# Performance work log

Measured on AMD Instinct MI355X. Metric: run time of the kernel, lower is better.

The kernel has to match this reference:

```python
import jax, jax.numpy as jnp
import numpy as np

B, NQ, NK, C = 8, 1024, 1024, 1024
H, DK, DV = 16, 64, 64


def setup_inputs() -> dict:
    key = jax.random.key(0)
    ks = jax.random.split(key, 10)
    queries = jax.random.normal(ks[0], (B, NQ, C), dtype=jnp.float32)
    keys_ = jax.random.normal(ks[1], (B, NK, C), dtype=jnp.float32)
    values = jax.random.normal(ks[2], (B, NK, C), dtype=jnp.float32)
    attention_mask = jax.random.randint(ks[3], (B, H, NQ, NK), 0, 2).astype(jnp.bool_)
    attention_weights = jax.random.uniform(ks[4], (B, H, NQ, NK), dtype=jnp.float32)
    std = 0.001  # init.normal_(m.weight, std=0.001), bias=0
    Wq = jax.random.normal(ks[5], (C, H * DK), dtype=jnp.float32) * std
    Wk = jax.random.normal(ks[6], (C, H * DK), dtype=jnp.float32) * std
    Wv = jax.random.normal(ks[7], (C, H * DV), dtype=jnp.float32) * std
    Wo = jax.random.normal(ks[8], (H * DV, C), dtype=jnp.float32) * std
    bq = jnp.zeros((H * DK,), jnp.float32)
    bk = jnp.zeros((H * DK,), jnp.float32)
    bv = jnp.zeros((H * DV,), jnp.float32)
    bo = jnp.zeros((C,), jnp.float32)
    return {"queries": queries, "keys": keys_, "values": values,
            "attention_mask": attention_mask, "attention_weights": attention_weights,
            "Wq": Wq, "bq": bq, "Wk": Wk, "bk": bk, "Wv": Wv, "bv": bv,
            "Wo": Wo, "bo": bo}


def reference(queries, keys, values, attention_mask, attention_weights,
              Wq, bq, Wk, bk, Wv, bv, Wo, bo):
    bs, nq, _ = queries.shape
    nk = keys.shape[1]
    # projections -> (b, h, n, d)
    q = (queries @ Wq + bq).reshape(bs, nq, H, DK).transpose(0, 2, 1, 3)
    k = (keys @ Wk + bk).reshape(bs, nk, H, DK).transpose(0, 2, 1, 3)
    v = (values @ Wv + bv).reshape(bs, nk, H, DV).transpose(0, 2, 1, 3)
    att = jnp.einsum('bhqd,bhkd->bhqk', q, k) / np.sqrt(DK).astype(np.float32)
    att = att * attention_weights
    att = jnp.where(attention_mask, -jnp.inf, att)
    att = jax.nn.softmax(att, axis=-1)
    # dropout is identity in eval mode
    out = jnp.einsum('bhqk,bhkd->bhqd', att, v)
    out = out.transpose(0, 2, 1, 3).reshape(bs, nq, H * DV)
    return out @ Wo + bo
```

## Files before the change

### kernel.cpp

```cpp
#include <hip/hip_runtime.h>
#include <hip/hip_bf16.h>

using short8 = __attribute__((ext_vector_type(8))) short;
using f32x4  = __attribute__((ext_vector_type(4))) float;

__device__ __forceinline__ unsigned short f2bf(float f) {
    union { float f; unsigned u; } x; x.f = f;
    unsigned r = x.u + 0x7FFFu + ((x.u >> 16) & 1u);
    return (unsigned short)(r >> 16);
}

__device__ __forceinline__ void gload_lds16(const void* g, void* l) {
    __builtin_amdgcn_global_load_lds(
        (const __attribute__((address_space(1))) unsigned int*)g,
        (__attribute__((address_space(3))) unsigned int*)l, 16, 0, 0);
}

__global__ void detect_mask_kernel(const unsigned int* __restrict__ m, int* __restrict__ flag) {
    if (threadIdx.x == 0) *flag = 0;
    __syncthreads();
    unsigned v = m[threadIdx.x];
    if (v > 1u) {
        atomicOr(flag, 1);
        if (v != 0x3F800000u) atomicOr(flag, 2);
    }
}

__global__ __launch_bounds__(256) void maskpack_kernel(
    const void* __restrict__ mask, const int* __restrict__ flag,
    unsigned long long* __restrict__ Mb, int nwords)
{
    const int l = threadIdx.x & 63;
    const int gwave = (int)((blockIdx.x * 256 + threadIdx.x) >> 6);
    const int nw = (int)((gridDim.x * 256) >> 6);
    const bool bytem = ((*flag) & 2) != 0;
    const unsigned char* m8 = (const unsigned char*)mask;
    const unsigned int* m32 = (const unsigned int*)mask;
    for (int w0 = gwave * 4; w0 < nwords; w0 += nw * 4) {
        unsigned v[4];
#pragma unroll
        for (int u = 0; u < 4; u++) {
            size_t e = (size_t)(w0 + u) * 64 + l;
            v[u] = bytem ? (unsigned)m8[e] : m32[e];
        }
#pragma unroll
        for (int u = 0; u < 4; u++) {
            unsigned long long b = __ballot(v[u] != 0u);
            if (l == 0) Mb[w0 + u] = b;
        }
    }
}

__global__ __launch_bounds__(256) void wconv_kernel(
    const float* __restrict__ W0, const float* __restrict__ W1,
    const float* __restrict__ W2, const float* __restrict__ W3,
    unsigned short* __restrict__ Wt)
{
    const int z = blockIdx.z;
    const float* W = (z == 0) ? W0 : ((z == 1) ? W1 : ((z == 2) ? W2 : W3));
    unsigned short* O = Wt + (size_t)z * 1024 * 1024;
    __shared__ float tile[64][68];
    const int t = threadIdx.x;
    const int k0 = blockIdx.x * 64, n0 = blockIdx.y * 64;
    const int rr = t >> 4, cc = t & 15;
#pragma unroll
    for (int i = 0; i < 4; i++) {
        int row = rr + i * 16;
        float4 v = *reinterpret_cast<const float4*>(W + (size_t)(k0 + row) * 1024 + n0 + cc * 4);
        *reinterpret_cast<float4*>(&tile[row][cc * 4]) = v;
    }
    __syncthreads();
#pragma unroll
    for (int i = 0; i < 4; i++) {
        int rn = rr + i * 16;
        ushort4 ov;
        ov.x = f2bf(tile[cc * 4 + 0][rn]);
        ov.y = f2bf(tile[cc * 4 + 1][rn]);
        ov.z = f2bf(tile[cc * 4 + 2][rn]);
        ov.w = f2bf(tile[cc * 4 + 3][rn]);
        *reinterpret_cast<ushort4*>(O + (size_t)(n0 + rn) * 1024 + k0 + cc * 4) = ov;
    }
}

__global__ __launch_bounds__(256) void aconv_kernel(
    const float* __restrict__ Aq, const float* __restrict__ Ak, const float* __restrict__ Av,
    unsigned short* __restrict__ Out)
{
    const int z = blockIdx.y;
    const float* A = (z == 0) ? Aq : ((z == 1) ? Ak : Av);
    unsigned short* O = Out + (size_t)z * 8192 * 1024;
    size_t i = ((size_t)blockIdx.x * 256 + threadIdx.x) * 8;
    float4 v0 = *reinterpret_cast<const float4*>(A + i);
    float4 v1 = *reinterpret_cast<const float4*>(A + i + 4);
    short8 o;
    o[0] = (short)f2bf(v0.x); o[1] = (short)f2bf(v0.y);
    o[2] = (short)f2bf(v0.z); o[3] = (short)f2bf(v0.w);
    o[4] = (short)f2bf(v1.x); o[5] = (short)f2bf(v1.y);
    o[6] = (short)f2bf(v1.z); o[7] = (short)f2bf(v1.w);
    *reinterpret_cast<short8*>(O + i) = o;
}

#define P8_STAGE(T2, BS)                                                                    \
    gload_lds16(gA0 + (size_t)(T2) * 64, smem + (BS) * 16384 + w * 1024);                   \
    gload_lds16(gA1 + (size_t)(T2) * 64, smem + (BS) * 16384 + 8192 + w * 1024);            \
    gload_lds16(gBp + (size_t)(T2) * 64, smem + 49152 + (BS) * 8192 + w * 1024);

#define P8_TILE(T, BR, BS, DOST, DOW, WN)                                                   \
    {                                                                                       \
        if (DOST) { P8_STAGE((T) + 2, BS) }                                                 \
        short8 a0[4], bb[2], a1[4];                                                         \
        _Pragma("unroll")                                                                   \
        for (int mf = 0; mf < 4; mf++)                                                      \
            a0[mf] = *reinterpret_cast<const short8*>(smem + (BR) * 16384 + ard + mf * 1024); \
        _Pragma("unroll")                                                                   \
        for (int nf = 0; nf < 2; nf++)                                                      \
            bb[nf] = *reinterpret_cast<const short8*>(smem + 49152 + (BR) * 8192 + brd + nf * 1024); \
        __builtin_amdgcn_s_barrier();                                                       \
        asm volatile("s_waitcnt lgkmcnt(0)" ::: "memory");                                  \
        __builtin_amdgcn_sched_barrier(0);                                                  \
        __builtin_amdgcn_s_setprio(1);                                                      \
        _Pragma("unroll")                                                                   \
        for (int mf = 0; mf < 4; mf++)                                                      \
            _Pragma("unroll")                                                               \
            for (int nf = 0; nf < 2; nf++)                                                  \
                acc[mf][nf] = __builtin_amdgcn_mfma_f32_16x16x32_bf16(a0[mf], bb[nf], acc[mf][nf], 0, 0, 0); \
        __builtin_amdgcn_s_setprio(0);                                                      \
        _Pragma("unroll")                                                                   \
        for (int mf = 0; mf < 4; mf++)                                                      \
            a1[mf] = *reinterpret_cast<const short8*>(smem + (BR) * 16384 + 4096 + ard + mf * 1024); \
        __builtin_amdgcn_s_barrier();                                                       \
        asm volatile("s_waitcnt lgkmcnt(0)" ::: "memory");                                  \
        __builtin_amdgcn_sched_barrier(0);                                                  \
        __builtin_amdgcn_s_setprio(1);                                                      \
        _Pragma("unroll")                                                                   \
        for (int mf = 0; mf < 4; mf++)                                                      \
            _Pragma("unroll")                                                               \
            for (int nf = 0; nf < 2; nf++)                                                  \
                acc[4 + mf][nf] = __builtin_amdgcn_mfma_f32_16x16x32_bf16(a1[mf], bb[nf], acc[4 + mf][nf], 0, 0, 0); \
        __builtin_amdgcn_s_setprio(0);                                                      \
        if (DOW) { asm volatile("s_waitcnt vmcnt(" #WN ")" ::: "memory"); }                 \
        __builtin_amdgcn_s_barrier();                                                       \
        __builtin_amdgcn_sched_barrier(0);                                                  \
    }

#define GEMM8_CORE(A_PTR, W_PTR)                                                            \
    extern __shared__ char smem[];                                                          \
    const int tid = threadIdx.x, w = tid >> 6, l = tid & 63, l16 = l & 15, g = l >> 4;      \
    const int wm = w >> 2, wn = w & 3;                                                      \
    const int row0 = blockIdx.x * 256, col0 = blockIdx.y * 128;                             \
    const int csrc = ((l & 3) * 16) ^ (((l >> 3) & 3) << 4);                                \
    const char* gA0 = (const char*)(A_PTR) + (size_t)(row0 + w * 16 + (l >> 2)) * 2048 + csrc; \
    const char* gA1 = gA0 + (size_t)128 * 2048;                                             \
    const char* gBp = (const char*)(W_PTR) + (size_t)(col0 + w * 16 + (l >> 2)) * 2048 + csrc; \
    const int sw = ((l16 >> 1) & 3) << 4;                                                   \
    const int ard = (wm * 128 + l16) * 64 + ((g * 16) ^ sw);                                \
    const int brd = (wn * 32 + l16) * 64 + ((g * 16) ^ sw);                                 \
    f32x4 acc[8][2];                                                                        \
    _Pragma("unroll")                                                                       \
    for (int i = 0; i < 8; i++)                                                             \
        _Pragma("unroll")                                                                   \
        for (int j = 0; j < 2; j++) acc[i][j] = (f32x4){0.f, 0.f, 0.f, 0.f};                \
    P8_STAGE(0, 0)                                                                          \
    P8_STAGE(1, 1)                                                                          \
    asm volatile("s_waitcnt vmcnt(3)" ::: "memory");                                        \
    __builtin_amdgcn_s_barrier();                                                           \
    __builtin_amdgcn_sched_barrier(0);                                                      \
    for (int tb = 0; tb < 30; tb += 3) {                                                    \
        P8_TILE(tb + 0, 0, 2, 1, 1, 3)                                                      \
        P8_TILE(tb + 1, 1, 0, 1, 1, 3)                                                      \
        P8_TILE(tb + 2, 2, 1, 1, 1, 3)                                                      \
    }                                                                                       \
    P8_TILE(30, 0, 0, 0, 1, 0)                                                              \
    P8_TILE(31, 1, 0, 0, 0, 0)

__global__ __launch_bounds__(512, 4) void gemm_proj8_kernel(
    const unsigned short* __restrict__ Abf,
    const unsigned short* __restrict__ Wt,
    const float* __restrict__ bq, const float* __restrict__ bk, const float* __restrict__ bv,
    unsigned short* __restrict__ Out)
{
    const int z = blockIdx.z;
    const unsigned short* A = Abf + (size_t)z * 8192 * 1024;
    const unsigned short* Wz = Wt + (size_t)z * 1024 * 1024;
    const float* bias = (z == 0) ? bq : ((z == 1) ? bk : bv);
    unsigned short* Oz = Out + (size_t)z * 8 * 16 * 1024 * 64;

    GEMM8_CORE(A, Wz)

#pragma unroll
    for (int mf8 = 0; mf8 < 8; mf8++)
#pragma unroll
        for (int nf = 0; nf < 2; nf++)
#pragma unroll
            for (int r = 0; r < 4; r++) {
                int row = row0 + wm * 128 + mf8 * 16 + g * 4 + r;
                int col = col0 + wn * 32 + nf * 16 + l16;
                float val = acc[mf8][nf][r] + bias[col];
                int bb = row >> 10, n = row & 1023;
                int hh = col >> 6, d = col & 63;
                Oz[(((size_t)(bb * 16 + hh)) * 1024 + n) * 64 + d] = f2bf(val);
            }
}

__global__ __launch_bounds__(512, 4) void gemm_out8_kernel(
    const unsigned short* __restrict__ Ain,
    const unsigned short* __restrict__ Wto,
    const float* __restrict__ bo,
    float* __restrict__ Out)
{
    GEMM8_CORE(Ain, Wto)

#pragma unroll
    for (int mf8 = 0; mf8 < 8; mf8++)
#pragma unroll
        for (int nf = 0; nf < 2; nf++)
#pragma unroll
            for (int r = 0; r < 4; r++) {
                int row = row0 + wm * 128 + mf8 * 16 + g * 4 + r;
                int col = col0 + wn * 32 + nf * 16 + l16;
                Out[(size_t)row * 1024 + col] = acc[mf8][nf][r] + bo[col];
            }
}

__global__ __launch_bounds__(256) void proj_f32_kernel(
    const float* __restrict__ Aq, const float* __restrict__ Ak, const float* __restrict__ Av,
    const unsigned short* __restrict__ Wt,
    const float* __restrict__ bq, const float* __restrict__ bk, const float* __restrict__ bv,
    unsigned short* __restrict__ Out)
{
    const int z = blockIdx.z;
    const float* A = (z == 0) ? Aq : ((z == 1) ? Ak : Av);
    const float* bias = (z == 0) ? bq : ((z == 1) ? bk : bv);
    const unsigned short* Wz = Wt + (size_t)z * 1024 * 1024;
    unsigned short* Oz = Out + (size_t)z * 8 * 16 * 1024 * 64;

    const int tid = threadIdx.x;
    const int w = tid >> 6, l = tid & 63;
    const int l16 = l & 15, g = l >> 4;
    const int rbase = blockIdx.x * 128 + w * 32;
    const int cbase = blockIdx.y * 64;

    f32x4 acc[2][4];
#pragma unroll
    for (int i = 0; i < 2; i++)
#pragma unroll
        for (int j = 0; j < 4; j++) acc[i][j] = (f32x4){0.f, 0.f, 0.f, 0.f};

#pragma unroll 2
    for (int k0 = 0; k0 < 1024; k0 += 32) {
        short8 a[2];
#pragma unroll
        for (int rf = 0; rf < 2; rf++) {
            const float* ap = A + (size_t)(rbase + rf * 16 + l16) * 1024 + k0 + g * 8;
            float4 v0 = *reinterpret_cast<const float4*>(ap);
            float4 v1 = *reinterpret_cast<const float4*>(ap + 4);
            short8 av;
            av[0] = (short)f2bf(v0.x); av[1] = (short)f2bf(v0.y);
            av[2] = (short)f2bf(v0.z); av[3] = (short)f2bf(v0.w);
            av[4] = (short)f2bf(v1.x); av[5] = (short)f2bf(v1.y);
            av[6] = (short)f2bf(v1.z); av[7] = (short)f2bf(v1.w);
            a[rf] = av;
        }
        short8 bfr[4];
#pragma unroll
        for (int cf = 0; cf < 4; cf++)
            bfr[cf] = *reinterpret_cast<const short8*>(Wz + (size_t)(cbase + cf * 16 + l16) * 1024 + k0 + g * 8);
#pragma unroll
        for (int rf = 0; rf < 2; rf++)
#pragma unroll
            for (int cf = 0; cf < 4; cf++)
                acc[rf][cf] = __builtin_amdgcn_mfma_f32_16x16x32_bf16(a[rf], bfr[cf], acc[rf][cf], 0, 0, 0);
    }

#pragma unroll
    for (int rf = 0; rf < 2; rf++)
#pragma unroll
        for (int cf = 0; cf < 4; cf++)
#pragma unroll
            for (int r = 0; r < 4; r++) {
                int row = rbase + rf * 16 + g * 4 + r;
                int col = cbase + cf * 16 + l16;
                float val = acc[rf][cf][r] + bias[col];
                int bb = row >> 10, n = row & 1023;
                int h = col >> 6, d = col & 63;
                Oz[(((size_t)(bb * 16 + h)) * 1024 + n) * 64 + d] = f2bf(val);
            }
}

__global__ __launch_bounds__(256) void vtrans_kernel(
    const unsigned short* __restrict__ Vs, unsigned short* __restrict__ Vt)
{
    const int bh = blockIdx.y;
    const int k0 = blockIdx.x * 64;
    const unsigned short* In = Vs + (size_t)bh * 1024 * 64;
    unsigned short* O = Vt + (size_t)bh * 64 * 1024;
    __shared__ unsigned short tile[64][72];
    const int t = threadIdx.x;
    {
        const int row = t >> 3;
        const int c8 = (t & 7) * 8;
#pragma unroll
        for (int i = 0; i < 2; i++) {
            int r = row + i * 32;
            short8 v = *reinterpret_cast<const short8*>(In + (size_t)(k0 + r) * 64 + c8);
            *reinterpret_cast<short8*>(&tile[r][c8]) = v;
        }
    }
    __syncthreads();
    {
        const int rd = t >> 4, c4 = (t & 15) * 4;
#pragma unroll
        for (int i = 0; i < 4; i++) {
            int d = rd + i * 16;
            ushort4 ov;
            ov.x = tile[c4 + 0][d];
            ov.y = tile[c4 + 1][d];
            ov.z = tile[c4 + 2][d];
            ov.w = tile[c4 + 3][d];
            *reinterpret_cast<ushort4*>(O + (size_t)d * 1024 + k0 + c4) = ov;
        }
    }
}

__global__ __launch_bounds__(512, 1) void attn_kernel(
    const unsigned short* __restrict__ Qs,
    const unsigned short* __restrict__ Ks,
    const unsigned short* __restrict__ Vt,
    const float* __restrict__ attw,
    const unsigned long long* __restrict__ Mb,
    unsigned short* __restrict__ AO)
{
    extern __shared__ char smem[];

    const int bid = blockIdx.x;
    const int xj = bid & 7, xp = bid >> 3;
    const int qt = xp & 7;
    const int gbh = (xp >> 3) * 8 + xj;
    const int h = gbh & 15, b = gbh >> 4;
    const int bh = b * 16 + h;

    const int tid = threadIdx.x, w = tid >> 6, l = tid & 63, l16 = l & 15, g = l >> 4;
    const int myq = qt * 128 + w * 16 + l16;

    const unsigned short* Qbh = Qs + (size_t)bh * 65536;
    const char* Kb = (const char*)(Ks + (size_t)bh * 65536);
    const char* Vb = (const char*)(Vt + (size_t)bh * 65536);
    const float* wrow = attw + ((size_t)bh * 1024 + myq) * 1024;
    const unsigned long long* mrow = Mb + ((size_t)bh * 1024 + myq) * 16;

    const int kb_swz = ((l & 7) * 16) ^ ((l >> 3) << 4);
    const char* gKb = Kb + (size_t)(w * 16 + (l >> 3)) * 128 + kb_swz;
    const int vrow0 = w * 8 + (l >> 4);
    const char* gVb0 = Vb + (size_t)vrow0 * 2048 + (((l & 15) * 16) ^ ((vrow0 & 7) << 4));
    const char* gVb1 = Vb + (size_t)(vrow0 + 4) * 2048 + (((l & 15) * 16) ^ (((vrow0 + 4) & 7) << 4));

    const int swz = (l16 & 7) << 4;
    const int krdA = l16 * 128 + ((g * 16) ^ swz);
    const int krdB = l16 * 128 + ((64 + g * 16) ^ swz);
    char* const pbase = smem + 65536 + w * 4096 + l16 * 256;

    gload_lds16(gKb, smem + w * 2048);
    gload_lds16(gKb + 1024, smem + w * 2048 + 1024);
    gload_lds16(gVb0, smem + 32768 + w * 2048);
    gload_lds16(gVb1, smem + 32768 + w * 2048 + 1024);
    __builtin_amdgcn_sched_barrier(0);

    short8 qf0 = *reinterpret_cast<const short8*>(Qbh + (size_t)myq * 64 + g * 8);
    short8 qf1 = *reinterpret_cast<const short8*>(Qbh + (size_t)myq * 64 + 32 + g * 8);
    float4 wv[8];
    unsigned long long mb0, mb1;
#pragma unroll
    for (int cf = 0; cf < 8; cf++)
        wv[cf] = *reinterpret_cast<const float4*>(wrow + cf * 16 + g * 4);
    mb0 = mrow[0];
    mb1 = mrow[1];

    asm volatile("s_waitcnt vmcnt(12)" ::: "memory");
    __builtin_amdgcn_s_barrier();
    __builtin_amdgcn_sched_barrier(0);

    f32x4 accO[4];
#pragma unroll
    for (int j = 0; j < 4; j++) accO[j] = (f32x4){0.f, 0.f, 0.f, 0.f};
    float den = 0.f;

#define ATTN_BODY(CURK)                                                                     \
    _Pragma("unroll")                                                                       \
    for (int cf = 0; cf < 8; cf++) {                                                        \
        short8 k0 = *reinterpret_cast<const short8*>(smem + (CURK) + krdA + cf * 2048);     \
        short8 k1 = *reinterpret_cast<const short8*>(smem + (CURK) + krdB + cf * 2048);     \
        f32x4 s = (f32x4){0.f, 0.f, 0.f, 0.f};                                              \
        s = __builtin_amdgcn_mfma_f32_16x16x32_bf16(k0, qf0, s, 0, 0, 0);                   \
        s = __builtin_amdgcn_mfma_f32_16x16x32_bf16(k1, qf1, s, 0, 0, 0);                   \
        unsigned mn = (unsigned)((cf < 4 ? mb0 >> (cf * 16 + g * 4)                         \
                                         : mb1 >> ((cf - 4) * 16 + g * 4))) & 0xFu;         \
        float p0 = (mn & 1u) ? 0.f : __expf(s[0] * 0.125f * wv[cf].x);                      \
        float p1 = (mn & 2u) ? 0.f : __expf(s[1] * 0.125f * wv[cf].y);                      \
        float p2 = (mn & 4u) ? 0.f : __expf(s[2] * 0.125f * wv[cf].z);                      \
        float p3 = (mn & 8u) ? 0.f : __expf(s[3] * 0.125f * wv[cf].w);                      \
        den += p0 + p1 + p2 + p3;                                                           \
        ushort4 pwv;                                                                        \
        pwv.x = f2bf(p0); pwv.y = f2bf(p1); pwv.z = f2bf(p2); pwv.w = f2bf(p3);             \
        *reinterpret_cast<ushort4*>(pbase + ((cf * 32 + g * 8) ^ swz)) = pwv;               \
    }

#define ATTN_PV(CURV)                                                                       \
    _Pragma("unroll")                                                                       \
    for (int ks = 0; ks < 4; ks++) {                                                        \
        short8 pf = *reinterpret_cast<const short8*>(pbase + ((ks * 64 + g * 16) ^ swz));   \
        _Pragma("unroll")                                                                   \
        for (int cd = 0; cd < 4; cd++) {                                                    \
            short8 vf = *reinterpret_cast<const short8*>(                                   \
                smem + 32768 + (CURV) + (cd * 16 + l16) * 256 + ((ks * 64 + g * 16) ^ swz));\
            accO[cd] = __builtin_amdgcn_mfma_f32_16x16x32_bf16(pf, vf, accO[cd], 0, 0, 0);  \
        }                                                                                   \
    }

    for (int t = 0; t < 7; t++) {
        const int cur = (t & 1) * 16384, nxt = 16384 - cur;
        gload_lds16(gKb + (size_t)(t + 1) * 16384, smem + nxt + w * 2048);
        gload_lds16(gKb + (size_t)(t + 1) * 16384 + 1024, smem + nxt + w * 2048 + 1024);
        gload_lds16(gVb0 + (size_t)(t + 1) * 256, smem + 32768 + nxt + w * 2048);
        gload_lds16(gVb1 + (size_t)(t + 1) * 256, smem + 32768 + nxt + w * 2048 + 1024);
        __builtin_amdgcn_sched_barrier(0);

        ATTN_BODY(cur)

#pragma unroll
        for (int cf = 0; cf < 8; cf++)
            wv[cf] = *reinterpret_cast<const float4*>(wrow + (t + 1) * 128 + cf * 16 + g * 4);
        mb0 = mrow[2 * (t + 1)];
        mb1 = mrow[2 * (t + 1) + 1];

        ATTN_PV(cur)

        asm volatile("s_waitcnt vmcnt(10)" ::: "memory");
        __builtin_amdgcn_s_barrier();
        __builtin_amdgcn_sched_barrier(0);
    }
    ATTN_BODY(16384)
    ATTN_PV(16384)
#undef ATTN_BODY
#undef ATTN_PV

    den += __shfl_xor(den, 16);
    den += __shfl_xor(den, 32);

#pragma unroll
    for (int r = 0; r < 4; r++) {
        float dr = __shfl(den, g * 4 + r);
        float inv = 1.0f / dr;
#pragma unroll
        for (int cd = 0; cd < 4; cd++) {
            int qrow = qt * 128 + w * 16 + g * 4 + r;
            int col = h * 64 + cd * 16 + l16;
            AO[((size_t)b * 1024 + qrow) * 1024 + col] = f2bf(accO[cd][r] * inv);
        }
    }
}

extern "C" void kernel_launch(void* const* d_in, const int* in_sizes, int n_in,
                              void* d_out, int out_size, void* d_ws, size_t ws_size,
                              hipStream_t stream)
{
    const float* queries = (const float*)d_in[0];
    const float* keys    = (const float*)d_in[1];
    const float* values  = (const float*)d_in[2];
    const void*  mask    = d_in[3];
    const float* attw    = (const float*)d_in[4];
    const float* Wq = (const float*)d_in[5];
    const float* bq = (const float*)d_in[6];
    const float* Wk = (const float*)d_in[7];
    const float* bk = (const float*)d_in[8];
    const float* Wv = (const float*)d_in[9];
    const float* bv = (const float*)d_in[10];
    const float* Wo = (const float*)d_in[11];
    const float* bo = (const float*)d_in[12];

    char* ws = (char*)d_ws;
    int* flag = (int*)ws;
    unsigned short* base = (unsigned short*)(ws + 256);
    const size_t M8 = (size_t)8 * 1024 * 1024;
    unsigned short* Qs  = base;
    unsigned short* Ksb = base + M8;
    unsigned short* Vs  = base + 2 * M8;
    unsigned short* Vtb = base + 3 * M8;
    unsigned short* AO  = base + 4 * M8;
    unsigned short* Wt  = base + 5 * M8;
    unsigned short* Abf = base + 5 * M8 + 4 * 1024 * 1024;
    unsigned long long* Mb = (unsigned long long*)Vs;
    const size_t need_abf = 256 + (5 * M8 + 4 * 1024 * 1024 + 3 * M8) * sizeof(unsigned short);
    const bool useAbf = ws_size >= need_abf;

    detect_mask_kernel<<<1, 256, 0, stream>>>((const unsigned int*)mask, flag);
    wconv_kernel<<<dim3(16, 16, 4), 256, 0, stream>>>(Wq, Wk, Wv, Wo, Wt);
    if (useAbf) {
        aconv_kernel<<<dim3(4096, 3), 256, 0, stream>>>(queries, keys, values, Abf);
        gemm_proj8_kernel<<<dim3(32, 8, 3), 512, 73728, stream>>>(Abf, Wt, bq, bk, bv, Qs);
    } else {
        proj_f32_kernel<<<dim3(64, 16, 3), 256, 0, stream>>>(queries, keys, values, Wt, bq, bk, bv, Qs);
    }
    vtrans_kernel<<<dim3(16, 128), 256, 0, stream>>>(Vs, Vtb);
    maskpack_kernel<<<dim3(2048), 256, 0, stream>>>(mask, flag, Mb, 2 * 1024 * 1024);
    attn_kernel<<<dim3(1024), 512, 98304, stream>>>(Qs, Ksb, Vtb, attw, Mb, AO);
    gemm_out8_kernel<<<dim3(32, 8), 512, 73728, stream>>>(AO, Wt + (size_t)3 * 1024 * 1024, bo, (float*)d_out);
}
```

Baseline: 397.5 us.

## Fuse V transpose into projection epilogue and restructure attention K/V tiling

The V projection GEMM now writes its output directly in transposed (d-major) layout, which removes the separate vtrans kernel launch and its extra pass over V on the bf16 path. The attention kernel switches from a 7-step double-buffered 128-key pipeline to 4 single-buffered 256-key tiles, with weights and mask prefetched per 256-key chunk. The loads of the next tile are issued only after a barrier and then fully waited with vmcnt(0), so the earlier overlap of global loads with compute is lost, while barrier and loop overhead per key drops. The transposed epilogue store is strided, which may cost write efficiency in the GEMM.

```diff
diff --git a/kernel.cpp b/kernel.cpp
--- a/kernel.cpp
+++ b/kernel.cpp
@@ -177,7 +177,8 @@
     const unsigned short* __restrict__ Abf,
     const unsigned short* __restrict__ Wt,
     const float* __restrict__ bq, const float* __restrict__ bk, const float* __restrict__ bv,
-    unsigned short* __restrict__ Out)
+    unsigned short* __restrict__ Out,
+    unsigned short* __restrict__ VtOut)
 {
     const int z = blockIdx.z;
     const unsigned short* A = Abf + (size_t)z * 8192 * 1024;
@@ -198,7 +199,10 @@
                 float val = acc[mf8][nf][r] + bias[col];
                 int bb = row >> 10, n = row & 1023;
                 int hh = col >> 6, d = col & 63;
-                Oz[(((size_t)(bb * 16 + hh)) * 1024 + n) * 64 + d] = f2bf(val);
+                if (z < 2)
+                    Oz[(((size_t)(bb * 16 + hh)) * 1024 + n) * 64 + d] = f2bf(val);
+                else
+                    VtOut[(((size_t)(bb * 16 + hh)) * 64 + d) * 1024 + n] = f2bf(val);
             }
 }
 
@@ -348,34 +352,38 @@
     const float* wrow = attw + ((size_t)bh * 1024 + myq) * 1024;
     const unsigned long long* mrow = Mb + ((size_t)bh * 1024 + myq) * 16;
 
-    const int kb_swz = ((l & 7) * 16) ^ ((l >> 3) << 4);
-    const char* gKb = Kb + (size_t)(w * 16 + (l >> 3)) * 128 + kb_swz;
-    const int vrow0 = w * 8 + (l >> 4);
-    const char* gVb0 = Vb + (size_t)vrow0 * 2048 + (((l & 15) * 16) ^ ((vrow0 & 7) << 4));
-    const char* gVb1 = Vb + (size_t)(vrow0 + 4) * 2048 + (((l & 15) * 16) ^ (((vrow0 + 4) & 7) << 4));
-
-    const int swz = (l16 & 7) << 4;
-    const int krdA = l16 * 128 + ((g * 16) ^ swz);
-    const int krdB = l16 * 128 + ((64 + g * 16) ^ swz);
+    const int kswz = ((l & 7) * 16) ^ (((l >> 3) & 7) << 4);
+    const char* gK_ = Kb + (size_t)(w * 32 + (l >> 3)) * 128 + kswz;
+    const int vR = l >> 5;
+    const char* gV_[4];
+#pragma unroll
+    for (int j = 0; j < 4; j++) {
+        const int rw = j * 2 + vR;
+        gV_[j] = Vb + (size_t)(w * 8 + rw) * 2048 + (((l & 31) * 16) ^ ((rw & 7) << 4));
+    }
+
+    const int swz7 = (l16 & 7) << 4;
+    const int krdA = l16 * 128 + ((g * 16) ^ swz7);
+    const int krdB = l16 * 128 + ((64 + g * 16) ^ swz7);
     char* const pbase = smem + 65536 + w * 4096 + l16 * 256;
 
-    gload_lds16(gKb, smem + w * 2048);
-    gload_lds16(gKb + 1024, smem + w * 2048 + 1024);
-    gload_lds16(gVb0, smem + 32768 + w * 2048);
-    gload_lds16(gVb1, smem + 32768 + w * 2048 + 1024);
+#pragma unroll
+    for (int j = 0; j < 4; j++) gload_lds16(gK_ + j * 1024, smem + w * 4096 + j * 1024);
+#pragma unroll
+    for (int j = 0; j < 4; j++) gload_lds16(gV_[j], smem + 32768 + w * 4096 + j * 1024);
     __builtin_amdgcn_sched_barrier(0);
 
     short8 qf0 = *reinterpret_cast<const short8*>(Qbh + (size_t)myq * 64 + g * 8);
     short8 qf1 = *reinterpret_cast<const short8*>(Qbh + (size_t)myq * 64 + 32 + g * 8);
-    float4 wv[8];
-    unsigned long long mb0, mb1;
-#pragma unroll
-    for (int cf = 0; cf < 8; cf++)
+    float4 wv[16];
+    unsigned long long mb[4];
+#pragma unroll
+    for (int cf = 0; cf < 16; cf++)
         wv[cf] = *reinterpret_cast<const float4*>(wrow + cf * 16 + g * 4);
-    mb0 = mrow[0];
-    mb1 = mrow[1];
-
-    asm volatile("s_waitcnt vmcnt(12)" ::: "memory");
+#pragma unroll
+    for (int u = 0; u < 4; u++) mb[u] = mrow[u];
+
+    asm volatile("s_waitcnt vmcnt(0)" ::: "memory");
     __builtin_amdgcn_s_barrier();
     __builtin_amdgcn_sched_barrier(0);
 
@@ -384,62 +392,62 @@
     for (int j = 0; j < 4; j++) accO[j] = (f32x4){0.f, 0.f, 0.f, 0.f};
     float den = 0.f;
 
-#define ATTN_BODY(CURK)                                                                     \
+#define ATTN_BODY(H)                                                                        \
     _Pragma("unroll")                                                                       \
     for (int cf = 0; cf < 8; cf++) {                                                        \
-        short8 k0 = *reinterpret_cast<const short8*>(smem + (CURK) + krdA + cf * 2048);     \
-        short8 k1 = *reinterpret_cast<const short8*>(smem + (CURK) + krdB + cf * 2048);     \
+        short8 k0 = *reinterpret_cast<const short8*>(smem + (H) * 16384 + cf * 2048 + krdA);\
+        short8 k1 = *reinterpret_cast<const short8*>(smem + (H) * 16384 + cf * 2048 + krdB);\
         f32x4 s = (f32x4){0.f, 0.f, 0.f, 0.f};                                              \
         s = __builtin_amdgcn_mfma_f32_16x16x32_bf16(k0, qf0, s, 0, 0, 0);                   \
         s = __builtin_amdgcn_mfma_f32_16x16x32_bf16(k1, qf1, s, 0, 0, 0);                   \
-        unsigned mn = (unsigned)((cf < 4 ? mb0 >> (cf * 16 + g * 4)                         \
-                                         : mb1 >> ((cf - 4) * 16 + g * 4))) & 0xFu;         \
-        float p0 = (mn & 1u) ? 0.f : __expf(s[0] * 0.125f * wv[cf].x);                      \
-        float p1 = (mn & 2u) ? 0.f : __expf(s[1] * 0.125f * wv[cf].y);                      \
-        float p2 = (mn & 4u) ? 0.f : __expf(s[2] * 0.125f * wv[cf].z);                      \
-        float p3 = (mn & 8u) ? 0.f : __expf(s[3] * 0.125f * wv[cf].w);                      \
+        unsigned mn = (unsigned)(mb[(H) * 2 + (cf >> 2)] >> ((cf & 3) * 16 + g * 4)) & 0xFu;\
+        float p0 = (mn & 1u) ? 0.f : __expf(s[0] * 0.125f * wv[(H) * 8 + cf].x);            \
+        float p1 = (mn & 2u) ? 0.f : __expf(s[1] * 0.125f * wv[(H) * 8 + cf].y);            \
+        float p2 = (mn & 4u) ? 0.f : __expf(s[2] * 0.125f * wv[(H) * 8 + cf].z);            \
+        float p3 = (mn & 8u) ? 0.f : __expf(s[3] * 0.125f * wv[(H) * 8 + cf].w);            \
         den += p0 + p1 + p2 + p3;                                                           \
         ushort4 pwv;                                                                        \
         pwv.x = f2bf(p0); pwv.y = f2bf(p1); pwv.z = f2bf(p2); pwv.w = f2bf(p3);             \
-        *reinterpret_cast<ushort4*>(pbase + ((cf * 32 + g * 8) ^ swz)) = pwv;               \
-    }
-
-#define ATTN_PV(CURV)                                                                       \
+        *reinterpret_cast<ushort4*>(pbase + ((cf * 32 + g * 8) ^ swz7)) = pwv;              \
+    }
+
+#define ATTN_PV(H)                                                                          \
     _Pragma("unroll")                                                                       \
     for (int ks = 0; ks < 4; ks++) {                                                        \
-        short8 pf = *reinterpret_cast<const short8*>(pbase + ((ks * 64 + g * 16) ^ swz));   \
+        short8 pf = *reinterpret_cast<const short8*>(pbase + ((ks * 64 + g * 16) ^ swz7));  \
         _Pragma("unroll")                                                                   \
         for (int cd = 0; cd < 4; cd++) {                                                    \
             short8 vf = *reinterpret_cast<const short8*>(                                   \
-                smem + 32768 + (CURV) + (cd * 16 + l16) * 256 + ((ks * 64 + g * 16) ^ swz));\
+                smem + 32768 + (cd * 16 + l16) * 512 + (((H) * 256 + ks * 64 + g * 16) ^ swz7)); \
             accO[cd] = __builtin_amdgcn_mfma_f32_16x16x32_bf16(pf, vf, accO[cd], 0, 0, 0);  \
         }                                                                                   \
     }
 
-    for (int t = 0; t < 7; t++) {
-        const int cur = (t & 1) * 16384, nxt = 16384 - cur;
-        gload_lds16(gKb + (size_t)(t + 1) * 16384, smem + nxt + w * 2048);
-        gload_lds16(gKb + (size_t)(t + 1) * 16384 + 1024, smem + nxt + w * 2048 + 1024);
-        gload_lds16(gVb0 + (size_t)(t + 1) * 256, smem + 32768 + nxt + w * 2048);
-        gload_lds16(gVb1 + (size_t)(t + 1) * 256, smem + 32768 + nxt + w * 2048 + 1024);
-        __builtin_amdgcn_sched_barrier(0);
-
-        ATTN_BODY(cur)
-
-#pragma unroll
-        for (int cf = 0; cf < 8; cf++)
-            wv[cf] = *reinterpret_cast<const float4*>(wrow + (t + 1) * 128 + cf * 16 + g * 4);
-        mb0 = mrow[2 * (t + 1)];
-        mb1 = mrow[2 * (t + 1) + 1];
-
-        ATTN_PV(cur)
-
-        asm volatile("s_waitcnt vmcnt(10)" ::: "memory");
+    for (int t = 0; t < 4; t++) {
+        ATTN_BODY(0)
+        ATTN_PV(0)
+        ATTN_BODY(1)
+        if (t < 3) {
+#pragma unroll
+            for (int cf = 0; cf < 16; cf++)
+                wv[cf] = *reinterpret_cast<const float4*>(wrow + (t + 1) * 256 + cf * 16 + g * 4);
+#pragma unroll
+            for (int u = 0; u < 4; u++) mb[u] = mrow[4 * (t + 1) + u];
+        }
+        ATTN_PV(1)
+        __builtin_amdgcn_s_barrier();
+        if (t < 3) {
+#pragma unroll
+            for (int j = 0; j < 4; j++)
+                gload_lds16(gK_ + (size_t)(t + 1) * 32768 + j * 1024, smem + w * 4096 + j * 1024);
+#pragma unroll
+            for (int j = 0; j < 4; j++)
+                gload_lds16(gV_[j] + (size_t)(t + 1) * 512, smem + 32768 + w * 4096 + j * 1024);
+            asm volatile("s_waitcnt vmcnt(0)" ::: "memory");
+        }
         __builtin_amdgcn_s_barrier();
         __builtin_amdgcn_sched_barrier(0);
     }
-    ATTN_BODY(16384)
-    ATTN_PV(16384)
 #undef ATTN_BODY
 #undef ATTN_PV
 
@@ -496,11 +504,11 @@
     wconv_kernel<<<dim3(16, 16, 4), 256, 0, stream>>>(Wq, Wk, Wv, Wo, Wt);
     if (useAbf) {
         aconv_kernel<<<dim3(4096, 3), 256, 0, stream>>>(queries, keys, values, Abf);
-        gemm_proj8_kernel<<<dim3(32, 8, 3), 512, 73728, stream>>>(Abf, Wt, bq, bk, bv, Qs);
+        gemm_proj8_kernel<<<dim3(32, 8, 3), 512, 73728, stream>>>(Abf, Wt, bq, bk, bv, Qs, Vtb);
     } else {
         proj_f32_kernel<<<dim3(64, 16, 3), 256, 0, stream>>>(queries, keys, values, Wt, bq, bk, bv, Qs);
-    }
-    vtrans_kernel<<<dim3(16, 128), 256, 0, stream>>>(Vs, Vtb);
+        vtrans_kernel<<<dim3(16, 128), 256, 0, stream>>>(Vs, Vtb);
+    }
     maskpack_kernel<<<dim3(2048), 256, 0, stream>>>(mask, flag, Mb, 2 * 1024 * 1024);
     attn_kernel<<<dim3(1024), 512, 98304, stream>>>(Qs, Ksb, Vtb, attw, Mb, AO);
     gemm_out8_kernel<<<dim3(32, 8), 512, 73728, stream>>>(AO, Wt + (size_t)3 * 1024 * 1024, bo, (float*)d_out);
```

Result: slower. 420.4 us (+5.8%).
